# Optimization experiments

Hardware: AMD Instinct MI355X
Metric: run time of the kernel (lower is better)

## Reference

```python
import jax, jax.numpy as jnp
import numpy as np

B = 4096
NUM_FEATURES = 40960
M = 256
N = 32
K = 1


def setup_inputs() -> dict:
    key = jax.random.key(0)
    ks = jax.random.split(key, 9)
    white = jax.random.uniform(ks[0], (B, NUM_FEATURES), dtype=jnp.float32)
    black = jax.random.uniform(ks[1], (B, NUM_FEATURES), dtype=jnp.float32)
    stm = jax.random.randint(ks[2], (B, 1), 0, 2).astype(jnp.float32)
    s_ft = 1.0 / np.sqrt(NUM_FEATURES)
    s_l1 = 1.0 / np.sqrt(2 * M)
    s_l2 = 1.0 / np.sqrt(N)
    ft_w = jax.random.uniform(ks[3], (M, NUM_FEATURES), jnp.float32, -s_ft, s_ft)
    ft_b = jax.random.uniform(ks[4], (M,), jnp.float32, -s_ft, s_ft)
    l1_w = jax.random.uniform(ks[5], (N, 2 * M), jnp.float32, -s_l1, s_l1)
    l1_b = jax.random.uniform(ks[6], (N,), jnp.float32, -s_l1, s_l1)
    l2_w = jax.random.uniform(ks[7], (K, N), jnp.float32, -s_l2, s_l2)
    l2_b = jax.random.uniform(ks[8], (K,), jnp.float32, -s_l2, s_l2)
    return {
        "white_features": white, "black_features": black, "stm": stm,
        "ft_w": ft_w, "ft_b": ft_b, "l1_w": l1_w, "l1_b": l1_b,
        "l2_w": l2_w, "l2_b": l2_b,
    }


def reference(white_features, black_features, stm, ft_w, ft_b, l1_w, l1_b, l2_w, l2_b):
    # feature transformer (embedding-bag style: sparse one-hot @ W^T)
    w = white_features @ ft_w.T + ft_b   # [B, M]
    b = black_features @ ft_w.T + ft_b   # [B, M]
    # stm-selected perspective concatenation
    acc = stm * jnp.concatenate([w, b], axis=1) + (1.0 - stm) * jnp.concatenate([b, w], axis=1)
    x = jnp.clip(acc, 0.0, 1.0)
    x = jnp.clip(x @ l1_w.T + l1_b, 0.0, 1.0)
    return x @ l2_w.T + l2_b  # [B, K]
```

## Files before the change

### kernel.cpp

```cpp
#include <hip/hip_runtime.h>
#include <hip/hip_bf16.h>
#include <stdint.h>

#define B_SZ   4096
#define F_SZ   40960
#define M_SZ   256
#define KSPLIT 4
#define KSLICE (F_SZ / KSPLIT)
#define BK     64
#define NCHUNK (KSLICE / BK)
#define AROWS  128
#define WR     256
#define LDT    72

typedef float    f32x4  __attribute__((ext_vector_type(4)));
typedef __bf16   bf16x4 __attribute__((ext_vector_type(4)));
typedef __bf16   bf16x8 __attribute__((ext_vector_type(8)));
typedef unsigned int u32x4 __attribute__((ext_vector_type(4)));

#define WS_WBF_BYTES ((size_t)M_SZ * F_SZ * 2)

__global__ __launch_bounds__(256) void k_wcvt(const float* __restrict__ src,
                                              __bf16* __restrict__ dst) {
    size_t i = ((size_t)blockIdx.x * 256 + threadIdx.x) * 8;
    f32x4 a = *(const f32x4*)(src + i);
    f32x4 b = *(const f32x4*)(src + i + 4);
    bf16x4 oa = __builtin_convertvector(a, bf16x4);
    bf16x4 ob = __builtin_convertvector(b, bf16x4);
    *(bf16x4*)(dst + i)     = oa;
    *(bf16x4*)(dst + i + 4) = ob;
}

__global__ __launch_bounds__(512, 2) void k_ftgemm(
    const float* __restrict__ white, const float* __restrict__ black,
    const __bf16* __restrict__ wbf, float* __restrict__ part)
{
    __shared__ __bf16 Abuf[AROWS * LDT];
    __shared__ __bf16 Wbuf[WR * LDT];

    const int tid   = threadIdx.x;
    const int r0    = blockIdx.x * 64;
    const int kbase = blockIdx.y * KSLICE;

    const int rw = tid >> 3;
    const int c8 = tid & 7;

    const float*  aW = white + (size_t)(r0 + rw) * F_SZ + kbase + c8 * 8;
    const float*  aB = black + (size_t)(r0 + rw) * F_SZ + kbase + c8 * 8;

    f32x4 areg[4];
    u32x4 wreg[4];

    const int lane = tid & 63;
    const int wv   = tid >> 6;
    const int m0   = (wv & 3) * 64;
    const int ar0  = (wv >> 2) * 64;
    const int lr   = lane & 15;
    const int q    = lane >> 4;

    f32x4 acc[4][4];
#pragma unroll
    for (int r = 0; r < 4; ++r)
#pragma unroll
        for (int c = 0; c < 4; ++c) acc[r][c] = (f32x4){0.f, 0.f, 0.f, 0.f};

    auto load_chunk = [&](int kc) {
        const int ko = kc * BK;
        areg[0] = *(const f32x4*)(aW + ko);
        areg[1] = *(const f32x4*)(aW + ko + 4);
        areg[2] = *(const f32x4*)(aB + ko);
        areg[3] = *(const f32x4*)(aB + ko + 4);
#pragma unroll
        for (int it = 0; it < 4; ++it)
            wreg[it] = *(const u32x4*)(wbf + (size_t)(rw + it * 64) * F_SZ
                                       + kbase + ko + c8 * 8);
    };

    load_chunk(0);

    for (int kc = 0; kc < NCHUNK; ++kc) {
        __syncthreads();
        {
            bf16x4 lo = __builtin_convertvector(areg[0], bf16x4);
            bf16x4 hi = __builtin_convertvector(areg[1], bf16x4);
            *(bf16x4*)&Abuf[rw * LDT + c8 * 8]     = lo;
            *(bf16x4*)&Abuf[rw * LDT + c8 * 8 + 4] = hi;
            lo = __builtin_convertvector(areg[2], bf16x4);
            hi = __builtin_convertvector(areg[3], bf16x4);
            *(bf16x4*)&Abuf[(64 + rw) * LDT + c8 * 8]     = lo;
            *(bf16x4*)&Abuf[(64 + rw) * LDT + c8 * 8 + 4] = hi;
#pragma unroll
            for (int it = 0; it < 4; ++it)
                *(u32x4*)&Wbuf[(rw + it * 64) * LDT + c8 * 8] = wreg[it];
        }
        __syncthreads();
        if (kc + 1 < NCHUNK) load_chunk(kc + 1);

#pragma unroll
        for (int kst = 0; kst < 2; ++kst) {
            bf16x8 af[4], wf[4];
#pragma unroll
            for (int r = 0; r < 4; ++r)
                af[r] = *(const bf16x8*)&Abuf[(ar0 + r * 16 + lr) * LDT + kst * 32 + q * 8];
#pragma unroll
            for (int c = 0; c < 4; ++c)
                wf[c] = *(const bf16x8*)&Wbuf[(m0 + c * 16 + lr) * LDT + kst * 32 + q * 8];
#pragma unroll
            for (int r = 0; r < 4; ++r)
#pragma unroll
                for (int c = 0; c < 4; ++c)
                    acc[r][c] = __builtin_amdgcn_mfma_f32_16x16x32_bf16(
                        af[r], wf[c], acc[r][c], 0, 0, 0);
        }
    }

    float* pbase = part + (size_t)blockIdx.y * ((size_t)B_SZ * 512);
#pragma unroll
    for (int r = 0; r < 4; ++r) {
        const int arow_base = ar0 + r * 16 + q * 4;
#pragma unroll
        for (int e = 0; e < 4; ++e) {
            const int arow  = arow_base + e;
            const int i     = r0 + (arow & 63);
            const int cbase = (arow >> 6) * 256 + m0;
#pragma unroll
            for (int c = 0; c < 4; ++c)
                pbase[(size_t)i * 512 + cbase + c * 16 + lr] = acc[r][c][e];
        }
    }
}

__global__ __launch_bounds__(256) void k_head(
    const float* __restrict__ part, const float* __restrict__ stm,
    const float* __restrict__ ftb,  const float* __restrict__ l1w,
    const float* __restrict__ l1b,  const float* __restrict__ l2w,
    const float* __restrict__ l2b,  float* __restrict__ out)
{
    __shared__ float xs[4][512];
    const int wv   = threadIdx.x >> 6;
    const int lane = threadIdx.x & 63;
    const int i    = blockIdx.x * 4 + wv;

    const int swap = (stm[i] == 0.0f) ? 256 : 0;

#pragma unroll
    for (int t = 0; t < 8; ++t) {
        const int j   = t * 64 + lane;
        const int col = (j + swap) & 511;
        float v = 0.f;
#pragma unroll
        for (int s = 0; s < KSPLIT; ++s)
            v += part[(size_t)s * B_SZ * 512 + (size_t)i * 512 + col];
        v += ftb[j & 255];
        v = fminf(fmaxf(v, 0.f), 1.f);
        xs[wv][j] = v;
    }
    __syncthreads();

    const int n = lane & 31;
    const int h = lane >> 5;
    float a = 0.f;
    const float* wrow = l1w + n * 512 + h * 256;
    const float* xrow = &xs[wv][h * 256];
#pragma unroll 8
    for (int jj = 0; jj < 256; jj += 4) {
        f32x4 xv = *(const f32x4*)(xrow + jj);
        f32x4 wv4 = *(const f32x4*)(wrow + jj);
        a += xv.x * wv4.x + xv.y * wv4.y + xv.z * wv4.z + xv.w * wv4.w;
    }
    a += __shfl_xor(a, 32);
    float y = fminf(fmaxf(a + l1b[n], 0.f), 1.f);

    float p = (h == 0) ? y * l2w[n] : 0.f;
#pragma unroll
    for (int off = 16; off >= 1; off >>= 1) p += __shfl_xor(p, off);
    if (lane == 0) out[i] = p + l2b[0];
}

extern "C" void kernel_launch(void* const* d_in, const int* in_sizes, int n_in,
                              void* d_out, int out_size, void* d_ws, size_t ws_size,
                              hipStream_t stream) {
    (void)in_sizes; (void)n_in; (void)out_size; (void)ws_size;
    const float* white = (const float*)d_in[0];
    const float* black = (const float*)d_in[1];
    const float* stm   = (const float*)d_in[2];
    const float* ftw   = (const float*)d_in[3];
    const float* ftb   = (const float*)d_in[4];
    const float* l1w   = (const float*)d_in[5];
    const float* l1b   = (const float*)d_in[6];
    const float* l2w   = (const float*)d_in[7];
    const float* l2b   = (const float*)d_in[8];

    __bf16* wbf = (__bf16*)d_ws;
    float*  part = (float*)((char*)d_ws + WS_WBF_BYTES);

    hipLaunchKernelGGL(k_wcvt, dim3((M_SZ * F_SZ) / (256 * 8)), dim3(256), 0, stream,
                       ftw, wbf);
    hipLaunchKernelGGL(k_ftgemm, dim3(B_SZ / 64, KSPLIT), dim3(512), 0, stream,
                       white, black, wbf, part);
    hipLaunchKernelGGL(k_head, dim3(B_SZ / 4), dim3(256), 0, stream,
                       part, stm, ftb, l1w, l1b, l2w, l2b, (float*)d_out);
}
```

Baseline: 1.409 ms.

## Stage bf16 weights via direct global-to-LDS loads with XOR swizzle and double buffering

```diff
diff --git a/kernel.cpp b/kernel.cpp
--- a/kernel.cpp
+++ b/kernel.cpp
@@ -9,102 +9,117 @@
 #define KSLICE (F_SZ / KSPLIT)
 #define BK     64
 #define NCHUNK (KSLICE / BK)
-#define AROWS  128
-#define WR     256
-#define LDT    72
 
 typedef float    f32x4  __attribute__((ext_vector_type(4)));
+typedef float    f32x8  __attribute__((ext_vector_type(8)));
 typedef __bf16   bf16x4 __attribute__((ext_vector_type(4)));
 typedef __bf16   bf16x8 __attribute__((ext_vector_type(8)));
-typedef unsigned int u32x4 __attribute__((ext_vector_type(4)));
 
 #define WS_WBF_BYTES ((size_t)M_SZ * F_SZ * 2)
+
+typedef const __attribute__((address_space(1))) unsigned int* gas_ptr;
+typedef __attribute__((address_space(3))) unsigned int*       las_ptr;
+__device__ __forceinline__ void gload_lds16(const void* g, void* l) {
+    __builtin_amdgcn_global_load_lds((gas_ptr)g, (las_ptr)l, 16, 0, 0);
+}
 
 __global__ __launch_bounds__(256) void k_wcvt(const float* __restrict__ src,
                                               __bf16* __restrict__ dst) {
-    size_t i = ((size_t)blockIdx.x * 256 + threadIdx.x) * 8;
-    f32x4 a = *(const f32x4*)(src + i);
-    f32x4 b = *(const f32x4*)(src + i + 4);
-    bf16x4 oa = __builtin_convertvector(a, bf16x4);
-    bf16x4 ob = __builtin_convertvector(b, bf16x4);
-    *(bf16x4*)(dst + i)     = oa;
-    *(bf16x4*)(dst + i + 4) = ob;
-}
-
-__global__ __launch_bounds__(512, 2) void k_ftgemm(
+    unsigned i = ((unsigned)blockIdx.x * 256 + threadIdx.x) * 8;
+    unsigned m   = i / F_SZ;
+    unsigned rem = i - m * F_SZ;
+    unsigned slot = (rem >> 3) & 7;
+    unsigned drem = (rem & ~63u) | ((slot ^ (m & 7)) << 3);
+    f32x8 a = *(const f32x8*)(src + i);
+    bf16x8 o = __builtin_convertvector(a, bf16x8);
+    *(bf16x8*)(dst + (size_t)m * F_SZ + drem) = o;
+}
+
+__global__ __launch_bounds__(256, 2) void k_ftgemm(
     const float* __restrict__ white, const float* __restrict__ black,
     const __bf16* __restrict__ wbf, float* __restrict__ part)
 {
-    __shared__ __bf16 Abuf[AROWS * LDT];
-    __shared__ __bf16 Wbuf[WR * LDT];
+    __shared__ __bf16 Abuf[64 * 64];
+    __shared__ __bf16 Wbuf[2][M_SZ * 64];
 
     const int tid   = threadIdx.x;
-    const int r0    = blockIdx.x * 64;
+    const int bx    = blockIdx.x;
+    const int persp = bx >> 6;
+    const int r0    = (bx & 63) * 64;
     const int kbase = blockIdx.y * KSLICE;
 
-    const int rw = tid >> 3;
-    const int c8 = tid & 7;
-
-    const float*  aW = white + (size_t)(r0 + rw) * F_SZ + kbase + c8 * 8;
-    const float*  aB = black + (size_t)(r0 + rw) * F_SZ + kbase + c8 * 8;
-
-    f32x4 areg[4];
-    u32x4 wreg[4];
+    const float* abase = persp ? black : white;
+
+    const int arw = tid >> 2;
+    const int as0 = (tid & 3) * 2;
+    const float* aP = abase + (size_t)(r0 + arw) * F_SZ + kbase + (tid & 3) * 16;
+    char* aW0 = (char*)Abuf + arw * 128 + (((as0    ) ^ (arw & 7)) << 4);
+    char* aW1 = (char*)Abuf + arw * 128 + (((as0 + 1) ^ (arw & 7)) << 4);
+
+    const __bf16* wPg = wbf + (size_t)(tid >> 3) * F_SZ + kbase + (tid & 7) * 8;
+
+    f32x8 areg[2];
+
+    auto load_A = [&](int kc) {
+        const float* p = aP + kc * BK;
+        areg[0] = *(const f32x8*)(p);
+        areg[1] = *(const f32x8*)(p + 8);
+    };
+    auto write_A = [&]() {
+        bf16x8 v0 = __builtin_convertvector(areg[0], bf16x8);
+        bf16x8 v1 = __builtin_convertvector(areg[1], bf16x8);
+        *(bf16x8*)aW0 = v0;
+        *(bf16x8*)aW1 = v1;
+    };
+    auto stage_W = [&](int kc, int buf) {
+        const __bf16* g = wPg + kc * BK;
+        char* l = (char*)&Wbuf[buf][0] + tid * 16;
+#pragma unroll
+        for (int c = 0; c < 8; ++c)
+            gload_lds16(g + (size_t)c * 32 * F_SZ, l + c * 4096);
+    };
 
     const int lane = tid & 63;
     const int wv   = tid >> 6;
-    const int m0   = (wv & 3) * 64;
-    const int ar0  = (wv >> 2) * 64;
+    const int m0   = wv * 64;
     const int lr   = lane & 15;
     const int q    = lane >> 4;
 
+    const int sw0 = (((q    ) ^ (lr & 7)) << 4);
+    const int sw1 = (((q | 4) ^ (lr & 7)) << 4);
+
+    const char* aR  = (const char*)Abuf + lr * 128;
+    const char* wR0 = (const char*)&Wbuf[0][0] + (m0 + lr) * 128;
+    const char* wR1 = (const char*)&Wbuf[1][0] + (m0 + lr) * 128;
+
     f32x4 acc[4][4];
 #pragma unroll
     for (int r = 0; r < 4; ++r)
 #pragma unroll
         for (int c = 0; c < 4; ++c) acc[r][c] = (f32x4){0.f, 0.f, 0.f, 0.f};
 
-    auto load_chunk = [&](int kc) {
-        const int ko = kc * BK;
-        areg[0] = *(const f32x4*)(aW + ko);
-        areg[1] = *(const f32x4*)(aW + ko + 4);
-        areg[2] = *(const f32x4*)(aB + ko);
-        areg[3] = *(const f32x4*)(aB + ko + 4);
-#pragma unroll
-        for (int it = 0; it < 4; ++it)
-            wreg[it] = *(const u32x4*)(wbf + (size_t)(rw + it * 64) * F_SZ
-                                       + kbase + ko + c8 * 8);
-    };
-
-    load_chunk(0);
+    stage_W(0, 0);
+    load_A(0);
 
     for (int kc = 0; kc < NCHUNK; ++kc) {
         __syncthreads();
-        {
-            bf16x4 lo = __builtin_convertvector(areg[0], bf16x4);
-            bf16x4 hi = __builtin_convertvector(areg[1], bf16x4);
-            *(bf16x4*)&Abuf[rw * LDT + c8 * 8]     = lo;
-            *(bf16x4*)&Abuf[rw * LDT + c8 * 8 + 4] = hi;
-            lo = __builtin_convertvector(areg[2], bf16x4);
-            hi = __builtin_convertvector(areg[3], bf16x4);
-            *(bf16x4*)&Abuf[(64 + rw) * LDT + c8 * 8]     = lo;
-            *(bf16x4*)&Abuf[(64 + rw) * LDT + c8 * 8 + 4] = hi;
-#pragma unroll
-            for (int it = 0; it < 4; ++it)
-                *(u32x4*)&Wbuf[(rw + it * 64) * LDT + c8 * 8] = wreg[it];
+        write_A();
+        __syncthreads();
+        if (kc + 1 < NCHUNK) {
+            stage_W(kc + 1, (kc + 1) & 1);
+            load_A(kc + 1);
         }
-        __syncthreads();
-        if (kc + 1 < NCHUNK) load_chunk(kc + 1);
-
+        const char* wR = (kc & 1) ? wR1 : wR0;
 #pragma unroll
         for (int kst = 0; kst < 2; ++kst) {
+            const int swk = kst ? sw1 : sw0;
             bf16x8 af[4], wf[4];
 #pragma unroll
             for (int r = 0; r < 4; ++r)
-                af[r] = *(const bf16x8*)&Abuf[(ar0 + r * 16 + lr) * LDT + kst * 32 + q * 8];
+                af[r] = *(const bf16x8*)(aR + r * 2048 + swk);
 #pragma unroll
             for (int c = 0; c < 4; ++c)
-                wf[c] = *(const bf16x8*)&Wbuf[(m0 + c * 16 + lr) * LDT + kst * 32 + q * 8];
+                wf[c] = *(const bf16x8*)(wR + c * 2048 + swk);
 #pragma unroll
             for (int r = 0; r < 4; ++r)
 #pragma unroll
@@ -114,20 +129,17 @@
         }
     }
 
-    float* pbase = part + (size_t)blockIdx.y * ((size_t)B_SZ * 512);
-#pragma unroll
-    for (int r = 0; r < 4; ++r) {
-        const int arow_base = ar0 + r * 16 + q * 4;
+    float* pb = part + (size_t)blockIdx.y * ((size_t)B_SZ * 512)
+              + (size_t)r0 * 512 + persp * 256 + m0;
+#pragma unroll
+    for (int r = 0; r < 4; ++r)
 #pragma unroll
         for (int e = 0; e < 4; ++e) {
-            const int arow  = arow_base + e;
-            const int i     = r0 + (arow & 63);
-            const int cbase = (arow >> 6) * 256 + m0;
+            const int row = r * 16 + q * 4 + e;
 #pragma unroll
             for (int c = 0; c < 4; ++c)
-                pbase[(size_t)i * 512 + cbase + c * 16 + lr] = acc[r][c][e];
+                pb[(size_t)row * 512 + c * 16 + lr] = acc[r][c][e];
         }
-    }
 }
 
 __global__ __launch_bounds__(256) void k_head(
@@ -164,7 +176,7 @@
     const float* xrow = &xs[wv][h * 256];
 #pragma unroll 8
     for (int jj = 0; jj < 256; jj += 4) {
-        f32x4 xv = *(const f32x4*)(xrow + jj);
+        f32x4 xv  = *(const f32x4*)(xrow + jj);
         f32x4 wv4 = *(const f32x4*)(wrow + jj);
         a += xv.x * wv4.x + xv.y * wv4.y + xv.z * wv4.z + xv.w * wv4.w;
     }
@@ -191,12 +203,12 @@
     const float* l2w   = (const float*)d_in[7];
     const float* l2b   = (const float*)d_in[8];
 
-    __bf16* wbf = (__bf16*)d_ws;
+    __bf16* wbf  = (__bf16*)d_ws;
     float*  part = (float*)((char*)d_ws + WS_WBF_BYTES);
 
     hipLaunchKernelGGL(k_wcvt, dim3((M_SZ * F_SZ) / (256 * 8)), dim3(256), 0, stream,
                        ftw, wbf);
-    hipLaunchKernelGGL(k_ftgemm, dim3(B_SZ / 64, KSPLIT), dim3(512), 0, stream,
+    hipLaunchKernelGGL(k_ftgemm, dim3(128, KSPLIT), dim3(256), 0, stream,
                        white, black, wbf, part);
     hipLaunchKernelGGL(k_head, dim3(B_SZ / 4), dim3(256), 0, stream,
                        part, stm, ftb, l1w, l1b, l2w, l2b, (float*)d_out);
```

New measurement: 1.435 ms. No clear change (+1.9%).
